# Optimization experiments

Measured on AMD Instinct MI355X. Metric: run time of the kernel, lower is better.

Reference implementation:

```python
import jax, jax.numpy as jnp
import numpy as np

# module hyper-parameters (init_kwargs)
DELTA_VAR = 0.75
DELTA_DIST = 2.0
ALPHA, BETA, GAMMA = 1.0, 1.0, 0.001

B, E, H, W, C = 4, 16, 512, 512, 24


def _safe_norm(x, axis):
    # L2 norm with zero (not nan) gradient at 0, matching torch.norm's subgradient
    sq = jnp.sum(x * x, axis=axis)
    safe = jnp.where(sq == 0, 1.0, sq)
    return jnp.where(sq == 0, 0.0, jnp.sqrt(safe))


def setup_inputs() -> dict:
    key = jax.random.key(0)
    k1, k2 = jax.random.split(key)
    input_ = jax.random.normal(k1, (B, E, H, W), dtype=jnp.float32)
    target = jax.random.randint(k2, (B, 1, H, W), 0, C)  # consecutive labels 0..C-1 (w.h.p. all present)
    return {"input_": input_, "target": target, "n_instances": C}


def reference(input_, target, n_instances):
    # Discriminative loss (De Brabandere et al. 2017), math identical to the torch
    # one-hot-expansion version but expressed as segment reductions + gathers.
    Cn = int(n_instances)
    b, e = input_.shape[0], input_.shape[1]
    emb = input_.reshape(b, e, -1).transpose(0, 2, 1)  # (B, N, E)
    tgt = target.reshape(b, -1)                        # (B, N) int labels

    # per-instance cluster means: segment-sum over pixels (the torch code does the
    # same reduction via a dense BxCxExHxW one-hot expansion)
    def _means(e_bn, t_n):
        sums = jax.ops.segment_sum(e_bn, t_n, num_segments=Cn)                      # (C, E)
        counts = jax.ops.segment_sum(jnp.ones(t_n.shape, e_bn.dtype), t_n, num_segments=Cn)  # (C,)
        return sums / counts[:, None], counts

    mu, counts = jax.vmap(_means)(emb, tgt)            # (B, C, E), (B, C)

    # variance term: hinged distance of each pixel embedding to its own cluster mean
    mu_per_pix = jnp.take_along_axis(mu, tgt[:, :, None], axis=1)  # (B, N, E)
    dist = _safe_norm(emb - mu_per_pix, axis=-1)                   # (B, N)
    hinge = jnp.square(jnp.maximum(dist - DELTA_VAR, 0.0))
    var_per_inst = jax.vmap(lambda h, t: jax.ops.segment_sum(h, t, num_segments=Cn))(hinge, tgt) / counts  # (B, C)
    variance_term = jnp.mean(jnp.sum(var_per_inst, axis=1) / Cn)

    # distance term: hinged pairwise repulsion between cluster means
    dmat = _safe_norm(mu[:, :, None, :] - mu[:, None, :, :], axis=-1)  # (B, C, C)
    repulsion = 2.0 * DELTA_DIST * (1.0 - jnp.eye(Cn, dtype=mu.dtype))
    hinged = jnp.square(jnp.maximum(repulsion - dmat, 0.0))
    distance_term = jnp.mean(jnp.sum(hinged, axis=(1, 2))) / (Cn * (Cn - 1))

    # regularizer: mean norm of cluster means
    reg_term = jnp.mean(jnp.sum(_safe_norm(mu, axis=-1), axis=1)) / Cn

    return ALPHA * variance_term + BETA * distance_term + GAMMA * reg_term
```

## Files before the change

kernel.cpp:

```cpp
#include <hip/hip_runtime.h>
#include <cstdint>

#define B_SZ   4
#define E_DIM  16
#define C_INST 24
#define HW_N   262144
#define NG     (HW_N / 4)

#define DELTA_VAR  0.75f
#define DELTA_DIST 2.0f
#define ALPHA_W 1.0f
#define BETA_W  1.0f
#define GAMMA_W 0.001f

#define P1_NB   32
#define P1_ITER (NG / (P1_NB * 256))
#define P2_TOTAL_BLOCKS (256 * B_SZ)

__global__ __launch_bounds__(256) void pass1_kernel(
    const float* __restrict__ input, const int* __restrict__ target,
    float* __restrict__ sums, float* __restrict__ counts)
{
    __shared__ float buk[256][25];
    __shared__ float crow[4][C_INST];
    const int tid  = threadIdx.x;
    const int lane = tid & 63;
    const int wv   = tid >> 6;
    const int chunk = blockIdx.x;
    const int eg    = blockIdx.y;
    const int b     = blockIdx.z;

    float* __restrict__ myrow = &buk[tid][0];
    #pragma unroll
    for (int j = 0; j < C_INST; ++j) myrow[j] = 0.f;

    const int4* __restrict__ tgt4 = (const int4*)(target + (size_t)b * HW_N);
    const float4* __restrict__ src4 =
        (const float4*)(input + ((size_t)b * E_DIM + eg) * HW_N);
    const int gbase = chunk * 256 * P1_ITER + tid;

    int scnt[C_INST];
    #pragma unroll
    for (int c = 0; c < C_INST; ++c) scnt[c] = 0;

    int4   lab = tgt4[gbase];
    float4 x   = src4[gbase];
    #pragma unroll
    for (int it = 0; it < P1_ITER; ++it) {
        const int4   lc = lab;
        const float4 xc = x;
        if (it + 1 < P1_ITER) {
            lab = tgt4[gbase + (it + 1) * 256];
            x   = src4[gbase + (it + 1) * 256];
        }
        myrow[lc.x] += xc.x;
        myrow[lc.y] += xc.y;
        myrow[lc.z] += xc.z;
        myrow[lc.w] += xc.w;
        if (eg < 8 && it == eg) {
            #pragma unroll
            for (int c = 0; c < C_INST; ++c) {
                scnt[c] += (int)__popcll(__ballot(lc.x == c))
                         + (int)__popcll(__ballot(lc.y == c))
                         + (int)__popcll(__ballot(lc.z == c))
                         + (int)__popcll(__ballot(lc.w == c));
            }
        }
    }
    if (lane == 0) {
        #pragma unroll
        for (int c = 0; c < C_INST; ++c) crow[wv][c] = (float)scnt[c];
    }
    __syncthreads();

    if (tid < 8 * C_INST) {
        const int c  = tid >> 3;
        const int r0 = tid & 7;
        float s = 0.f;
        #pragma unroll
        for (int i = 0; i < 32; ++i) s += buk[8 * i + r0][c];
        s += __shfl_xor(s, 1, 64);
        s += __shfl_xor(s, 2, 64);
        s += __shfl_xor(s, 4, 64);
        if (r0 == 0)
            unsafeAtomicAdd(&sums[((size_t)b * E_DIM + eg) * C_INST + c], s);
    }
    if (eg < 8 && tid < C_INST) {
        const float s = crow[0][tid] + crow[1][tid] + crow[2][tid] + crow[3][tid];
        unsafeAtomicAdd(&counts[b * C_INST + tid], s);
    }
}

__global__ __launch_bounds__(256) void pass2_kernel(
    const float* __restrict__ input, const int* __restrict__ target,
    const float* __restrict__ sums, const float* __restrict__ counts,
    float* __restrict__ partials)
{
    __shared__ float mu_l[C_INST][17];
    __shared__ float w_l[C_INST];
    __shared__ float redw[4];
    const int tid  = threadIdx.x;
    const int lane = tid & 63;
    const int wv   = tid >> 6;
    const int b    = blockIdx.y;

    if (tid < C_INST) {
        const float cv = counts[b * C_INST + tid];
        w_l[tid] = (cv > 0.f) ? 1.f / cv : 0.f;
    }
    __syncthreads();
    for (int i = tid; i < E_DIM * C_INST; i += 256) {
        const int e = i / C_INST, c = i % C_INST;
        mu_l[c][e] = sums[((size_t)b * E_DIM + e) * C_INST + c] * w_l[c];
    }
    __syncthreads();

    const int g = blockIdx.x * 256 + tid;
    const int4 lab4 = ((const int4*)(target + (size_t)b * HW_N))[g];
    const float4* __restrict__ src4 =
        (const float4*)(input + (size_t)b * E_DIM * HW_N);

    float4 xv[E_DIM];
    #pragma unroll
    for (int e = 0; e < E_DIM; ++e)
        xv[e] = src4[(size_t)e * NG + g];

    float d2[4] = {0.f, 0.f, 0.f, 0.f};
    #pragma unroll
    for (int e = 0; e < E_DIM; ++e) {
        float df;
        df = xv[e].x - mu_l[lab4.x][e]; d2[0] = fmaf(df, df, d2[0]);
        df = xv[e].y - mu_l[lab4.y][e]; d2[1] = fmaf(df, df, d2[1]);
        df = xv[e].z - mu_l[lab4.z][e]; d2[2] = fmaf(df, df, d2[2]);
        df = xv[e].w - mu_l[lab4.w][e]; d2[3] = fmaf(df, df, d2[3]);
    }

    float vloc = 0.f;
    {
        const int lp[4] = {lab4.x, lab4.y, lab4.z, lab4.w};
        #pragma unroll
        for (int p = 0; p < 4; ++p) {
            const float h = fmaxf(sqrtf(d2[p]) - DELTA_VAR, 0.f);
            vloc = fmaf(h * h, w_l[lp[p]], vloc);
        }
    }
    #pragma unroll
    for (int m = 1; m < 64; m <<= 1) vloc += __shfl_xor(vloc, m, 64);
    if (lane == 0) redw[wv] = vloc;
    __syncthreads();
    if (tid == 0)
        partials[b * 256 + blockIdx.x] = redw[0] + redw[1] + redw[2] + redw[3];
}

__global__ __launch_bounds__(256) void final_kernel(
    const float* __restrict__ sums, const float* __restrict__ counts,
    const float* __restrict__ partials, float* __restrict__ out)
{
    __shared__ float mu[B_SZ][C_INST][E_DIM];
    __shared__ float red[256];
    const int tid = threadIdx.x;

    for (int i = tid; i < B_SZ * C_INST * E_DIM; i += 256) {
        const int b = i / (C_INST * E_DIM);
        const int r = i % (C_INST * E_DIM);
        const int e = r / C_INST, c = r % C_INST;
        const float cv = counts[b * C_INST + c];
        mu[b][c][e] = (cv > 0.f)
            ? sums[((size_t)b * E_DIM + e) * C_INST + c] / cv : 0.f;
    }
    __syncthreads();

    float acc = 0.f;
    #pragma unroll
    for (int i = 0; i < P2_TOTAL_BLOCKS / 256; ++i)
        acc += partials[i * 256 + tid] * (ALPHA_W / (B_SZ * C_INST));
    for (int i = tid; i < B_SZ * C_INST; i += 256) {
        const int b = i / C_INST, c = i % C_INST;
        float n2 = 0.f;
        #pragma unroll
        for (int e = 0; e < E_DIM; ++e) n2 += mu[b][c][e] * mu[b][c][e];
        acc += GAMMA_W * sqrtf(n2) * (1.0f / (B_SZ * C_INST));
    }
    for (int i = tid; i < B_SZ * C_INST * C_INST; i += 256) {
        const int b  = i / (C_INST * C_INST);
        const int r  = i % (C_INST * C_INST);
        const int c1 = r / C_INST, c2 = r % C_INST;
        if (c1 != c2) {
            float d2 = 0.f;
            #pragma unroll
            for (int e = 0; e < E_DIM; ++e) {
                const float d = mu[b][c1][e] - mu[b][c2][e];
                d2 += d * d;
            }
            const float h = fmaxf(2.0f * DELTA_DIST - sqrtf(d2), 0.f);
            acc += BETA_W * h * h * (1.0f / (B_SZ * C_INST * (C_INST - 1)));
        }
    }

    red[tid] = acc;
    __syncthreads();
    for (int s = 128; s > 0; s >>= 1) {
        if (tid < s) red[tid] += red[tid + s];
        __syncthreads();
    }
    if (tid == 0) out[0] = red[0];
}

extern "C" void kernel_launch(void* const* d_in, const int* in_sizes, int n_in,
                              void* d_out, int out_size, void* d_ws, size_t ws_size,
                              hipStream_t stream)
{
    const float* input  = (const float*)d_in[0];
    const int*   target = (const int*)d_in[1];

    float* sums     = (float*)d_ws;
    float* counts   = sums + B_SZ * E_DIM * C_INST;
    float* partials = counts + B_SZ * C_INST;
    const size_t ws_zero_bytes =
        (size_t)(B_SZ * E_DIM * C_INST + B_SZ * C_INST) * sizeof(float);
    hipMemsetAsync(d_ws, 0, ws_zero_bytes, stream);

    pass1_kernel<<<dim3(P1_NB, E_DIM, B_SZ), 256, 0, stream>>>(input, target, sums, counts);
    pass2_kernel<<<dim3(256, B_SZ), 256, 0, stream>>>(input, target, sums, counts, partials);
    final_kernel<<<1, 256, 0, stream>>>(sums, counts, partials, (float*)d_out);
}
```

Before: 121.5 us.

## Fuse final reduction into pass2 via last-block ticket and drop memset

Pass1 now writes per-chunk partial sums into private slots instead of atomically accumulating into zeroed buffers. Counts come from an extra 'ones' plane instead of ballot/popcount work in some blocks. The separate final kernel is folded into pass2: a ticket counter picks the last block, which runs the distance and regularizer reduction. This removes the memset and one launch. In exchange, every pass2 block re-reduces 32 chunk partials per entry. The ticket relies on modular wraparound of a workspace counter that is never explicitly zeroed.

After: 250.7 us. 106% more time.

```diff
diff --git a/kernel.cpp b/kernel.cpp
--- a/kernel.cpp
+++ b/kernel.cpp
@@ -15,17 +15,16 @@
 
 #define P1_NB   32
 #define P1_ITER (NG / (P1_NB * 256))
-#define P2_TOTAL_BLOCKS (256 * B_SZ)
+#define NPLANE  (E_DIM + 1)
+#define P2_BX   256
+#define P2_TOTAL (P2_BX * B_SZ)
 
 __global__ __launch_bounds__(256) void pass1_kernel(
     const float* __restrict__ input, const int* __restrict__ target,
-    float* __restrict__ sums, float* __restrict__ counts)
+    float* __restrict__ sums_p)
 {
     __shared__ float buk[256][25];
-    __shared__ float crow[4][C_INST];
-    const int tid  = threadIdx.x;
-    const int lane = tid & 63;
-    const int wv   = tid >> 6;
+    const int tid   = threadIdx.x;
     const int chunk = blockIdx.x;
     const int eg    = blockIdx.y;
     const int b     = blockIdx.z;
@@ -34,42 +33,27 @@
     #pragma unroll
     for (int j = 0; j < C_INST; ++j) myrow[j] = 0.f;
 
+    const bool cntPlane = (eg == E_DIM);
     const int4* __restrict__ tgt4 = (const int4*)(target + (size_t)b * HW_N);
-    const float4* __restrict__ src4 =
-        (const float4*)(input + ((size_t)b * E_DIM + eg) * HW_N);
+    const float4* __restrict__ src4 = cntPlane ? (const float4*)nullptr
+        : (const float4*)(input + ((size_t)b * E_DIM + eg) * HW_N);
     const int gbase = chunk * 256 * P1_ITER + tid;
 
-    int scnt[C_INST];
-    #pragma unroll
-    for (int c = 0; c < C_INST; ++c) scnt[c] = 0;
-
     int4   lab = tgt4[gbase];
-    float4 x   = src4[gbase];
+    float4 x   = make_float4(1.f, 1.f, 1.f, 1.f);
+    if (!cntPlane) x = src4[gbase];
     #pragma unroll
     for (int it = 0; it < P1_ITER; ++it) {
         const int4   lc = lab;
         const float4 xc = x;
         if (it + 1 < P1_ITER) {
             lab = tgt4[gbase + (it + 1) * 256];
-            x   = src4[gbase + (it + 1) * 256];
-        }
-        myrow[lc.x] += xc.x;
-        myrow[lc.y] += xc.y;
-        myrow[lc.z] += xc.z;
-        myrow[lc.w] += xc.w;
-        if (eg < 8 && it == eg) {
-            #pragma unroll
-            for (int c = 0; c < C_INST; ++c) {
-                scnt[c] += (int)__popcll(__ballot(lc.x == c))
-                         + (int)__popcll(__ballot(lc.y == c))
-                         + (int)__popcll(__ballot(lc.z == c))
-                         + (int)__popcll(__ballot(lc.w == c));
-            }
-        }
-    }
-    if (lane == 0) {
-        #pragma unroll
-        for (int c = 0; c < C_INST; ++c) crow[wv][c] = (float)scnt[c];
+            if (!cntPlane) x = src4[gbase + (it + 1) * 256];
+        }
+        atomicAdd(&myrow[lc.x], xc.x);
+        atomicAdd(&myrow[lc.y], xc.y);
+        atomicAdd(&myrow[lc.z], xc.z);
+        atomicAdd(&myrow[lc.w], xc.w);
     }
     __syncthreads();
 
@@ -83,35 +67,41 @@
         s += __shfl_xor(s, 2, 64);
         s += __shfl_xor(s, 4, 64);
         if (r0 == 0)
-            unsafeAtomicAdd(&sums[((size_t)b * E_DIM + eg) * C_INST + c], s);
-    }
-    if (eg < 8 && tid < C_INST) {
-        const float s = crow[0][tid] + crow[1][tid] + crow[2][tid] + crow[3][tid];
-        unsafeAtomicAdd(&counts[b * C_INST + tid], s);
+            sums_p[(((size_t)b * NPLANE + eg) * P1_NB + chunk) * C_INST + c] = s;
     }
 }
 
 __global__ __launch_bounds__(256) void pass2_kernel(
     const float* __restrict__ input, const int* __restrict__ target,
-    const float* __restrict__ sums, const float* __restrict__ counts,
-    float* __restrict__ partials)
+    const float* __restrict__ sums_p, float* __restrict__ partials,
+    unsigned int* __restrict__ ticket, float* __restrict__ out)
 {
     __shared__ float mu_l[C_INST][17];
     __shared__ float w_l[C_INST];
     __shared__ float redw[4];
+    __shared__ float muF[B_SZ][C_INST][E_DIM];
+    __shared__ float red[256];
+    __shared__ int   lastFlag;
     const int tid  = threadIdx.x;
     const int lane = tid & 63;
     const int wv   = tid >> 6;
     const int b    = blockIdx.y;
 
     if (tid < C_INST) {
-        const float cv = counts[b * C_INST + tid];
+        float cv = 0.f;
+        #pragma unroll
+        for (int k = 0; k < P1_NB; ++k)
+            cv += sums_p[(((size_t)b * NPLANE + E_DIM) * P1_NB + k) * C_INST + tid];
         w_l[tid] = (cv > 0.f) ? 1.f / cv : 0.f;
     }
     __syncthreads();
     for (int i = tid; i < E_DIM * C_INST; i += 256) {
         const int e = i / C_INST, c = i % C_INST;
-        mu_l[c][e] = sums[((size_t)b * E_DIM + e) * C_INST + c] * w_l[c];
+        float s = 0.f;
+        #pragma unroll
+        for (int k = 0; k < P1_NB; ++k)
+            s += sums_p[(((size_t)b * NPLANE + e) * P1_NB + k) * C_INST + c];
+        mu_l[c][e] = s * w_l[c];
     }
     __syncthreads();
 
@@ -148,51 +138,56 @@
     for (int m = 1; m < 64; m <<= 1) vloc += __shfl_xor(vloc, m, 64);
     if (lane == 0) redw[wv] = vloc;
     __syncthreads();
-    if (tid == 0)
-        partials[b * 256 + blockIdx.x] = redw[0] + redw[1] + redw[2] + redw[3];
-}
-
-__global__ __launch_bounds__(256) void final_kernel(
-    const float* __restrict__ sums, const float* __restrict__ counts,
-    const float* __restrict__ partials, float* __restrict__ out)
-{
-    __shared__ float mu[B_SZ][C_INST][E_DIM];
-    __shared__ float red[256];
-    const int tid = threadIdx.x;
+
+    if (tid == 0) {
+        const float p = redw[0] + redw[1] + redw[2] + redw[3];
+        __hip_atomic_store(&partials[b * P2_BX + blockIdx.x], p,
+                           __ATOMIC_RELEASE, __HIP_MEMORY_SCOPE_AGENT);
+        const unsigned int old = __hip_atomic_fetch_add(
+            ticket, 1u, __ATOMIC_ACQ_REL, __HIP_MEMORY_SCOPE_AGENT);
+        lastFlag = (((old + 1u) & (P2_TOTAL - 1u)) == 0u);
+    }
+    __syncthreads();
+    if (!lastFlag) return;
 
     for (int i = tid; i < B_SZ * C_INST * E_DIM; i += 256) {
-        const int b = i / (C_INST * E_DIM);
-        const int r = i % (C_INST * E_DIM);
-        const int e = r / C_INST, c = r % C_INST;
-        const float cv = counts[b * C_INST + c];
-        mu[b][c][e] = (cv > 0.f)
-            ? sums[((size_t)b * E_DIM + e) * C_INST + c] / cv : 0.f;
+        const int bb = i / (C_INST * E_DIM);
+        const int r  = i % (C_INST * E_DIM);
+        const int e  = r / C_INST, c = r % C_INST;
+        float s = 0.f, cv = 0.f;
+        #pragma unroll
+        for (int k = 0; k < P1_NB; ++k) {
+            s  += sums_p[(((size_t)bb * NPLANE + e)     * P1_NB + k) * C_INST + c];
+            cv += sums_p[(((size_t)bb * NPLANE + E_DIM) * P1_NB + k) * C_INST + c];
+        }
+        muF[bb][c][e] = (cv > 0.f) ? s / cv : 0.f;
     }
     __syncthreads();
 
     float acc = 0.f;
-    #pragma unroll
-    for (int i = 0; i < P2_TOTAL_BLOCKS / 256; ++i)
-        acc += partials[i * 256 + tid] * (ALPHA_W / (B_SZ * C_INST));
+    for (int i = tid; i < P2_TOTAL; i += 256)
+        acc += __hip_atomic_load(&partials[i], __ATOMIC_ACQUIRE,
+                                 __HIP_MEMORY_SCOPE_AGENT)
+               * (ALPHA_W / (B_SZ * C_INST));
     for (int i = tid; i < B_SZ * C_INST; i += 256) {
-        const int b = i / C_INST, c = i % C_INST;
+        const int bb = i / C_INST, c = i % C_INST;
         float n2 = 0.f;
         #pragma unroll
-        for (int e = 0; e < E_DIM; ++e) n2 += mu[b][c][e] * mu[b][c][e];
+        for (int e = 0; e < E_DIM; ++e) n2 += muF[bb][c][e] * muF[bb][c][e];
         acc += GAMMA_W * sqrtf(n2) * (1.0f / (B_SZ * C_INST));
     }
     for (int i = tid; i < B_SZ * C_INST * C_INST; i += 256) {
-        const int b  = i / (C_INST * C_INST);
+        const int bb = i / (C_INST * C_INST);
         const int r  = i % (C_INST * C_INST);
         const int c1 = r / C_INST, c2 = r % C_INST;
         if (c1 != c2) {
-            float d2 = 0.f;
+            float dd = 0.f;
             #pragma unroll
             for (int e = 0; e < E_DIM; ++e) {
-                const float d = mu[b][c1][e] - mu[b][c2][e];
-                d2 += d * d;
+                const float d = muF[bb][c1][e] - muF[bb][c2][e];
+                dd += d * d;
             }
-            const float h = fmaxf(2.0f * DELTA_DIST - sqrtf(d2), 0.f);
+            const float h = fmaxf(2.0f * DELTA_DIST - sqrtf(dd), 0.f);
             acc += BETA_W * h * h * (1.0f / (B_SZ * C_INST * (C_INST - 1)));
         }
     }
@@ -213,14 +208,11 @@
     const float* input  = (const float*)d_in[0];
     const int*   target = (const int*)d_in[1];
 
-    float* sums     = (float*)d_ws;
-    float* counts   = sums + B_SZ * E_DIM * C_INST;
-    float* partials = counts + B_SZ * C_INST;
-    const size_t ws_zero_bytes =
-        (size_t)(B_SZ * E_DIM * C_INST + B_SZ * C_INST) * sizeof(float);
-    hipMemsetAsync(d_ws, 0, ws_zero_bytes, stream);
-
-    pass1_kernel<<<dim3(P1_NB, E_DIM, B_SZ), 256, 0, stream>>>(input, target, sums, counts);
-    pass2_kernel<<<dim3(256, B_SZ), 256, 0, stream>>>(input, target, sums, counts, partials);
-    final_kernel<<<1, 256, 0, stream>>>(sums, counts, partials, (float*)d_out);
+    float* sums_p   = (float*)d_ws;
+    float* partials = sums_p + (size_t)B_SZ * NPLANE * P1_NB * C_INST;
+    unsigned int* ticket = (unsigned int*)(partials + P2_TOTAL);
+
+    pass1_kernel<<<dim3(P1_NB, NPLANE, B_SZ), 256, 0, stream>>>(input, target, sums_p);
+    pass2_kernel<<<dim3(P2_BX, B_SZ), 256, 0, stream>>>(input, target, sums_p,
+                                                        partials, ticket, (float*)d_out);
 }
```
